# Kernel optimization log

Measured on AMD Instinct MI355X. Metric: run time of the kernel, lower is better.

## Reference

```python
import jax, jax.numpy as jnp
import numpy as np

TEMPERATURE = 0.07
NORM_EPS = 1e-12   # F.normalize eps
LOG_EPS = 1e-08


def setup_inputs() -> dict:
    key = jax.random.key(0)
    k1, k2 = jax.random.split(key)
    N, D, C = 8192, 512, 64
    projections = jax.random.normal(k1, (N, D), dtype=jnp.float32)
    targets = jax.random.randint(k2, (N,), 0, C, dtype=jnp.int64)
    return {"projections": projections, "targets": targets}


def reference(projections, targets):
    # L2-normalize rows (matches F.normalize: x / max(||x||, eps))
    norm = jnp.linalg.norm(projections, axis=1, keepdims=True)
    p = projections / jnp.maximum(norm, NORM_EPS)

    # [N, N] cosine similarity / temperature
    sim = jnp.matmul(p, p.T) / TEMPERATURE
    # row-max subtraction for numerical stability (gradient flows through max,
    # as in the torch original)
    sim = sim - jnp.max(sim, axis=1, keepdims=True)
    exp_sim = jnp.exp(sim)

    n = projections.shape[0]
    eye = jnp.eye(n, dtype=bool)
    mask_self = ~eye                                   # exclude self-pairs
    mask_pos = (targets[:, None] == targets[None, :]) & mask_self

    denom = jnp.sum(jnp.where(mask_self, exp_sim, 0.0), axis=1, keepdims=True)
    log_prob = sim - jnp.log(denom + LOG_EPS)

    num = jnp.sum(jnp.where(mask_pos, log_prob, 0.0), axis=1)
    cnt = jnp.sum(mask_pos, axis=1).astype(log_prob.dtype)
    # divide_no_nan: 0 where cnt == 0
    loss_per_sample = jnp.where(cnt == 0, 0.0, num / jnp.where(cnt == 0, 1.0, cnt))
    return loss_per_sample
```

## Files before the change

kernel.cpp:

```cpp
#include <hip/hip_runtime.h>
#include <hip/hip_bf16.h>
#include <math.h>

#define N_ROWS 8192
#define DIM    512
#define NCLS   64
#define BM     256
#define BK     64
#define NKT    (DIM / BK)
#define NTILE  (N_ROWS / BM)
#define NTRI   (NTILE * (NTILE + 1) / 2)
#define M_CONST 14.285714285714286f
#define SCALE_SQRT 3.7796447300922722f

using bf16x8 = __attribute__((ext_vector_type(8))) short;
using f32x4  = __attribute__((ext_vector_type(4))) float;

static __device__ inline unsigned short f2bf(float x) {
  unsigned u = __float_as_uint(x);
  unsigned r = u + 0x7FFFu + ((u >> 16) & 1u);
  return (unsigned short)(r >> 16);
}

__global__ __launch_bounds__(256) void normalize_rows(const float* __restrict__ proj,
                                                      unsigned short* __restrict__ outb) {
  const int row  = blockIdx.x * 4 + (threadIdx.x >> 6);
  const int lane = threadIdx.x & 63;
  const float4* src = (const float4*)(proj + (size_t)row * DIM);
  float4 a = src[lane * 2];
  float4 b = src[lane * 2 + 1];
  float ss = a.x*a.x + a.y*a.y + a.z*a.z + a.w*a.w
           + b.x*b.x + b.y*b.y + b.z*b.z + b.w*b.w;
#pragma unroll
  for (int off = 1; off < 64; off <<= 1) ss += __shfl_xor(ss, off);
  const float scale = SCALE_SQRT / fmaxf(sqrtf(ss), 1e-12f);
  float v[8] = {a.x, a.y, a.z, a.w, b.x, b.y, b.z, b.w};
  unsigned short h[8];
#pragma unroll
  for (int i = 0; i < 8; ++i) h[i] = f2bf(v[i] * scale);
  uint4 packed;
  packed.x = (unsigned)h[0] | ((unsigned)h[1] << 16);
  packed.y = (unsigned)h[2] | ((unsigned)h[3] << 16);
  packed.z = (unsigned)h[4] | ((unsigned)h[5] << 16);
  packed.w = (unsigned)h[6] | ((unsigned)h[7] << 16);
  *(uint4*)(outb + (size_t)row * DIM + lane * 8) = packed;
}

__global__ __launch_bounds__(1024) void class_hist(const int* __restrict__ tgt,
                                                   int* __restrict__ hist) {
  __shared__ int h[16][NCLS];
  const int wid = threadIdx.x >> 6;
  const int lane = threadIdx.x & 63;
  if (lane < NCLS) h[wid][lane] = 0;
  __syncthreads();
  for (int i = threadIdx.x; i < N_ROWS; i += 1024) atomicAdd(&h[wid][tgt[i]], 1);
  __syncthreads();
  if (threadIdx.x < NCLS) {
    int s = 0;
#pragma unroll
    for (int w = 0; w < 16; ++w) s += h[w][threadIdx.x];
    hist[threadIdx.x] = s;
  }
}

__global__ __launch_bounds__(512, 2) void supcon_tile(const unsigned short* __restrict__ p16,
                                                      const int* __restrict__ tgt,
                                                      float* __restrict__ dpart,
                                                      float* __restrict__ spart) {
  const int logical = ((int)blockIdx.x & 7) * (NTRI / 8) + ((int)blockIdx.x >> 3);
  int rem = logical, br = 0;
  while (rem >= NTILE - br) { rem -= NTILE - br; ++br; }
  const int bc = br + rem;

  __shared__ short As[2][BM * BK];
  __shared__ short Bs[2][BM * BK];
  __shared__ int   tgr[BM], tgc[BM];
  __shared__ float redE[4][BM], redS[4][BM];
  __shared__ float redEc[2][BM], redSc[2][BM];

  const int tid  = threadIdx.x;
  const int lane = tid & 63;
  const int wid  = tid >> 6;
  const int wm = wid >> 2, wn = wid & 3;
  const int lhi = lane >> 4, llo = lane & 15;

  const size_t rowA0 = (size_t)br * BM;
  const size_t rowB0 = (size_t)bc * BM;

#define STAGE_HALF(XS, BUF, ROW0, H, KT) do {                                   \
  _Pragma("unroll")                                                             \
  for (int j = 0; j < 2; ++j) {                                                 \
    const int g  = wid * 64 + lane + j * 512;                                   \
    const int r  = (H) * 128 + (g >> 3);                                        \
    const int gl = (g & 7) ^ (r & 7);                                           \
    const unsigned short* src = p16 + ((ROW0) + r) * DIM + (KT) * BK + gl * 8;  \
    __builtin_amdgcn_global_load_lds(                                           \
        (const __attribute__((address_space(1))) void*)src,                     \
        (__attribute__((address_space(3))) void*)&XS[BUF][(H) * 8192 + g * 8],  \
        16, 0, 0);                                                              \
  }                                                                             \
} while (0)

  STAGE_HALF(As, 0, rowA0, 0, 0);
  STAGE_HALF(As, 0, rowA0, 1, 0);
  STAGE_HALF(Bs, 0, rowB0, 0, 0);
  STAGE_HALF(Bs, 0, rowB0, 1, 0);
  if (tid < BM) tgr[tid] = tgt[br * BM + tid];
  else          tgc[tid - BM] = tgt[bc * BM + (tid - BM)];

  f32x4 zero = {0.f, 0.f, 0.f, 0.f};
  f32x4 acc[8][4];
#pragma unroll
  for (int i = 0; i < 8; ++i)
#pragma unroll
    for (int j = 0; j < 4; ++j) acc[i][j] = zero;

  __syncthreads();

  int cur = 0;
  for (int kt = 0; kt < NKT; ++kt) {
    const int nxt = cur ^ 1;
    const bool pf = (kt + 1 < NKT);

    bf16x8 bfr[4][2];
#pragma unroll
    for (int ni = 0; ni < 4; ++ni)
#pragma unroll
      for (int ks = 0; ks < 2; ++ks) {
        const int Rb = wn * 64 + ni * 16 + llo;
        bfr[ni][ks] = *(const bf16x8*)&Bs[cur][Rb * BK + (((ks * 4 + lhi) ^ (Rb & 7)) * 8)];
      }

#pragma unroll
    for (int ph = 0; ph < 4; ++ph) {
      const int h = ph >> 1, ks = ph & 1;
      bf16x8 af[4];
#pragma unroll
      for (int mi = 0; mi < 4; ++mi) {
        const int Ra = wm * 128 + h * 64 + mi * 16 + llo;
        af[mi] = *(const bf16x8*)&As[cur][Ra * BK + (((ks * 4 + lhi) ^ (Ra & 7)) * 8)];
      }
      if (pf) {
        if (ph == 0)      STAGE_HALF(As, nxt, rowA0, 0, kt + 1);
        else if (ph == 1) STAGE_HALF(As, nxt, rowA0, 1, kt + 1);
        else if (ph == 2) STAGE_HALF(Bs, nxt, rowB0, 0, kt + 1);
        else              STAGE_HALF(Bs, nxt, rowB0, 1, kt + 1);
      }
      __builtin_amdgcn_s_barrier();
      __builtin_amdgcn_s_setprio(1);
#pragma unroll
      for (int mi = 0; mi < 4; ++mi)
#pragma unroll
        for (int ni = 0; ni < 4; ++ni)
          acc[h * 4 + mi][ni] =
              __builtin_amdgcn_mfma_f32_16x16x32_bf16(af[mi], bfr[ni][ks], acc[h * 4 + mi][ni], 0, 0, 0);
      __builtin_amdgcn_s_setprio(0);
      if (ph < 3) __builtin_amdgcn_s_barrier();
    }
    __syncthreads();
    cur = nxt;
  }
#undef STAGE_HALF

  const bool diag = (br == bc);
  float ecol[4] = {0.f, 0.f, 0.f, 0.f};
  float scol[4] = {0.f, 0.f, 0.f, 0.f};

#pragma unroll
  for (int mi = 0; mi < 8; ++mi) {
#pragma unroll
    for (int rg = 0; rg < 4; ++rg) {
      const int rin  = wm * 128 + mi * 16 + lhi * 4 + rg;
      const int trow = tgr[rin];
      float esum = 0.f, ssum = 0.f;
#pragma unroll
      for (int ni = 0; ni < 4; ++ni) {
        const int cin = wn * 64 + ni * 16 + llo;
        const float sim = acc[mi][ni][rg];
        const bool self = diag && (rin == cin);
        const float e = self ? 0.f : __expf(sim - M_CONST);
        const bool pos = (!self) && (trow == tgc[cin]);
        const float sv = pos ? sim : 0.f;
        esum += e;  ssum += sv;
        ecol[ni] += e;  scol[ni] += sv;
      }
#pragma unroll
      for (int off = 1; off < 16; off <<= 1) {
        esum += __shfl_xor(esum, off);
        ssum += __shfl_xor(ssum, off);
      }
      if (llo == 0) { redE[wn][rin] = esum; redS[wn][rin] = ssum; }
    }
  }
  if (!diag) {
#pragma unroll
    for (int ni = 0; ni < 4; ++ni) {
      float ec = ecol[ni], sc = scol[ni];
      ec += __shfl_xor(ec, 16); ec += __shfl_xor(ec, 32);
      sc += __shfl_xor(sc, 16); sc += __shfl_xor(sc, 32);
      if (lhi == 0) {
        redEc[wm][wn * 64 + ni * 16 + llo] = ec;
        redSc[wm][wn * 64 + ni * 16 + llo] = sc;
      }
    }
  }
  __syncthreads();

  if (tid < BM) {
    const float e = redE[0][tid] + redE[1][tid] + redE[2][tid] + redE[3][tid];
    const float s = redS[0][tid] + redS[1][tid] + redS[2][tid] + redS[3][tid];
    dpart[(size_t)bc * N_ROWS + rowA0 + tid] = e;
    spart[(size_t)bc * N_ROWS + rowA0 + tid] = s;
  } else if (!diag) {
    const int c = tid - BM;
    dpart[(size_t)br * N_ROWS + rowB0 + c] = redEc[0][c] + redEc[1][c];
    spart[(size_t)br * N_ROWS + rowB0 + c] = redSc[0][c] + redSc[1][c];
  }
}

__global__ __launch_bounds__(256) void combine_loss(const float* __restrict__ dpart,
                                                    const float* __restrict__ spart,
                                                    const int* __restrict__ tgt,
                                                    const int* __restrict__ hist,
                                                    float* __restrict__ out) {
  __shared__ float dsh[4][64], ssh[4][64];
  const int lane = threadIdx.x & 63;
  const int g    = threadIdx.x >> 6;
  const int r    = blockIdx.x * 64 + lane;
  float d = 0.f, s = 0.f;
  for (int k = g * 8; k < g * 8 + 8; ++k) {
    d += dpart[(size_t)k * N_ROWS + r];
    s += spart[(size_t)k * N_ROWS + r];
  }
  dsh[g][lane] = d; ssh[g][lane] = s;
  __syncthreads();
  if (g == 0) {
    d = dsh[0][lane] + dsh[1][lane] + dsh[2][lane] + dsh[3][lane];
    s = ssh[0][lane] + ssh[1][lane] + ssh[2][lane] + ssh[3][lane];
    const int cnt = hist[tgt[r]] - 1;
    out[r] = (cnt > 0) ? (s / (float)cnt - M_CONST - logf(d + 1e-8f)) : 0.f;
  }
}

extern "C" void kernel_launch(void* const* d_in, const int* in_sizes, int n_in,
                              void* d_out, int out_size, void* d_ws, size_t ws_size,
                              hipStream_t stream) {
  const float* proj = (const float*)d_in[0];
  const int*   tgt  = (const int*)d_in[1];
  float* out = (float*)d_out;

  char* ws = (char*)d_ws;
  unsigned short* p16  = (unsigned short*)ws;
  float* dpart = (float*)(ws + (size_t)8 * 1024 * 1024);
  float* spart = (float*)(ws + (size_t)9 * 1024 * 1024);
  int*   hist  = (int*)(ws + (size_t)10 * 1024 * 1024);

  normalize_rows<<<N_ROWS / 4, 256, 0, stream>>>(proj, p16);
  class_hist<<<1, 1024, 0, stream>>>(tgt, hist);
  supcon_tile<<<NTRI, 512, 0, stream>>>(p16, tgt, dpart, spart);
  combine_loss<<<N_ROWS / 64, 256, 0, stream>>>(dpart, spart, tgt, hist, out);
}
```

Measured before the change: 101.4 us.

## Restructure GEMM K-loop prefetch with whole-tile staging and explicit vmcnt waits

The next K-tile is now issued in full at the top of each iteration instead of being split across the four compute phases. Explicit `s_waitcnt vmcnt`/`lgkmcnt` waits and `sched_barrier` fences replace the `__syncthreads` plus paired per-phase barriers, and the K-loop is fully unrolled. The aim is to cut barrier count and give the global-to-LDS loads a whole iteration to land behind MFMA work. It depends on hand-counted outstanding-load numbers staying right, and full unrolling may raise register pressure. The combine loop bound is rewritten in terms of a slot constant with the same value.

After: 105.1 us. 1.04x slower.

```diff
diff --git a/kernel.cpp b/kernel.cpp
--- a/kernel.cpp
+++ b/kernel.cpp
@@ -10,6 +10,7 @@
 #define NKT    (DIM / BK)
 #define NTILE  (N_ROWS / BM)
 #define NTRI   (NTILE * (NTILE + 1) / 2)
+#define NSLOT  NTILE
 #define M_CONST 14.285714285714286f
 #define SCALE_SQRT 3.7796447300922722f
 
@@ -101,12 +102,17 @@
   }                                                                             \
 } while (0)
 
-  STAGE_HALF(As, 0, rowA0, 0, 0);
-  STAGE_HALF(As, 0, rowA0, 1, 0);
-  STAGE_HALF(Bs, 0, rowB0, 0, 0);
-  STAGE_HALF(Bs, 0, rowB0, 1, 0);
-  if (tid < BM) tgr[tid] = tgt[br * BM + tid];
-  else          tgc[tid - BM] = tgt[bc * BM + (tid - BM)];
+#define STAGE_TILE(BUF, KT) do {          \
+  STAGE_HALF(As, BUF, rowA0, 0, KT);      \
+  STAGE_HALF(As, BUF, rowA0, 1, KT);      \
+  STAGE_HALF(Bs, BUF, rowB0, 0, KT);      \
+  STAGE_HALF(Bs, BUF, rowB0, 1, KT);      \
+} while (0)
+
+  const int tg0 = (tid < BM) ? tgt[br * BM + tid] : tgt[bc * BM + (tid - BM)];
+  STAGE_TILE(0, 0);
+  if (tid < BM) tgr[tid] = tg0;
+  else          tgc[tid - BM] = tg0;
 
   f32x4 zero = {0.f, 0.f, 0.f, 0.f};
   f32x4 acc[8][4];
@@ -115,12 +121,19 @@
 #pragma unroll
     for (int j = 0; j < 4; ++j) acc[i][j] = zero;
 
-  __syncthreads();
-
-  int cur = 0;
+#pragma unroll
   for (int kt = 0; kt < NKT; ++kt) {
-    const int nxt = cur ^ 1;
-    const bool pf = (kt + 1 < NKT);
+    const int cur = kt & 1, nxt = cur ^ 1;
+
+    if (kt + 1 < NKT) {
+      STAGE_TILE(nxt, kt + 1);
+      asm volatile("s_waitcnt vmcnt(8)");
+    } else {
+      asm volatile("s_waitcnt vmcnt(0)");
+    }
+    __builtin_amdgcn_sched_barrier(0);
+    __builtin_amdgcn_s_barrier();
+    __builtin_amdgcn_sched_barrier(0);
 
     bf16x8 bfr[4][2];
 #pragma unroll
@@ -140,13 +153,8 @@
         const int Ra = wm * 128 + h * 64 + mi * 16 + llo;
         af[mi] = *(const bf16x8*)&As[cur][Ra * BK + (((ks * 4 + lhi) ^ (Ra & 7)) * 8)];
       }
-      if (pf) {
-        if (ph == 0)      STAGE_HALF(As, nxt, rowA0, 0, kt + 1);
-        else if (ph == 1) STAGE_HALF(As, nxt, rowA0, 1, kt + 1);
-        else if (ph == 2) STAGE_HALF(Bs, nxt, rowB0, 0, kt + 1);
-        else              STAGE_HALF(Bs, nxt, rowB0, 1, kt + 1);
-      }
-      __builtin_amdgcn_s_barrier();
+      asm volatile("s_waitcnt lgkmcnt(0)");
+      __builtin_amdgcn_sched_barrier(0);
       __builtin_amdgcn_s_setprio(1);
 #pragma unroll
       for (int mi = 0; mi < 4; ++mi)
@@ -155,11 +163,10 @@
           acc[h * 4 + mi][ni] =
               __builtin_amdgcn_mfma_f32_16x16x32_bf16(af[mi], bfr[ni][ks], acc[h * 4 + mi][ni], 0, 0, 0);
       __builtin_amdgcn_s_setprio(0);
-      if (ph < 3) __builtin_amdgcn_s_barrier();
-    }
-    __syncthreads();
-    cur = nxt;
-  }
+      __builtin_amdgcn_s_barrier();
+    }
+  }
+#undef STAGE_TILE
 #undef STAGE_HALF
 
   const bool diag = (br == bc);
@@ -228,7 +235,7 @@
   const int g    = threadIdx.x >> 6;
   const int r    = blockIdx.x * 64 + lane;
   float d = 0.f, s = 0.f;
-  for (int k = g * 8; k < g * 8 + 8; ++k) {
+  for (int k = g * (NSLOT / 4); k < (g + 1) * (NSLOT / 4); ++k) {
     d += dpart[(size_t)k * N_ROWS + r];
     s += spart[(size_t)k * N_ROWS + r];
   }
```
